# Kernel optimization log

Hardware: AMD Instinct MI355X
Metric: run time of the kernel (lower is better)

The kernel has to match this reference:

```python
import jax, jax.numpy as jnp
import numpy as np

DIM = 1024
HEADS = 16
HEAD_DIM = DIM // HEADS
LAYERS = 8
HIDDEN = 4 * DIM
VOCAB = 266
MAX_POS = 32768
B = 4
L = 2048
SCALE = HEAD_DIM ** -0.5
EPS = 1e-5


def layer_norm(x, g, b):
    m = jnp.mean(x, axis=-1, keepdims=True)
    v = jnp.mean(jnp.square(x - m), axis=-1, keepdims=True)
    return (x - m) * jax.lax.rsqrt(v + EPS) * g + b


def setup_inputs() -> dict:
    key = jax.random.key(0)
    ks = jax.random.split(key, 16)
    s = 0.02
    return {
        "tokens": jax.random.randint(ks[0], (B, L), 0, VOCAB),
        "tok_emb": jax.random.normal(ks[1], (VOCAB, DIM), jnp.float32) * s,
        "pos_emb": jax.random.normal(ks[2], (MAX_POS, DIM), jnp.float32) * s,
        "ln1_g": jnp.ones((LAYERS, DIM), jnp.float32),
        "ln1_b": jnp.zeros((LAYERS, DIM), jnp.float32),
        "q_w": jax.random.normal(ks[3], (LAYERS, DIM, DIM), jnp.float32) * s,
        "k_w": jax.random.normal(ks[4], (LAYERS, DIM, DIM), jnp.float32) * s,
        "v_w": jax.random.normal(ks[5], (LAYERS, DIM, DIM), jnp.float32) * s,
        "o_w": jax.random.normal(ks[6], (LAYERS, DIM, DIM), jnp.float32) * s,
        "ln2_g": jnp.ones((LAYERS, DIM), jnp.float32),
        "ln2_b": jnp.zeros((LAYERS, DIM), jnp.float32),
        "w1_w": jax.random.normal(ks[7], (LAYERS, HIDDEN, DIM), jnp.float32) * s,
        "wg_w": jax.random.normal(ks[8], (LAYERS, HIDDEN, DIM), jnp.float32) * s,
        "w2_w": jax.random.normal(ks[9], (LAYERS, DIM, HIDDEN), jnp.float32) * s,
        "lnf_g": jnp.ones((DIM,), jnp.float32),
        "lnf_b": jnp.zeros((DIM,), jnp.float32),
        "lm_w": jax.random.normal(ks[10], (VOCAB, DIM), jnp.float32) * s,
    }


def reference(tokens, tok_emb, pos_emb, ln1_g, ln1_b, q_w, k_w, v_w, o_w,
              ln2_g, ln2_b, w1_w, wg_w, w2_w, lnf_g, lnf_b, lm_w):
    Bv, Lv = tokens.shape
    x = tok_emb[tokens] + pos_emb[jnp.arange(Lv)][None, :, :]  # [B,L,D]
    # strictly-upper-triangular causal mask (True = masked)
    rows = jnp.arange(Lv)
    mask = rows[None, :] > rows[:, None]  # [L,L], col > row
    pos_bias = jnp.arange(Lv, dtype=x.dtype) * 0.01  # [L]
    neg_inf = jnp.array(-jnp.inf, dtype=x.dtype)

    for i in range(LAYERS):
        h = layer_norm(x, ln1_g[i], ln1_b[i])
        q = jnp.einsum('bld,ed->ble', h, q_w[i]).reshape(Bv, Lv, HEADS, HEAD_DIM).transpose(0, 2, 1, 3)
        k = jnp.einsum('bld,ed->ble', h, k_w[i]).reshape(Bv, Lv, HEADS, HEAD_DIM).transpose(0, 2, 1, 3)
        v = jnp.einsum('bld,ed->ble', h, v_w[i]).reshape(Bv, Lv, HEADS, HEAD_DIM).transpose(0, 2, 1, 3)
        attn = jnp.einsum('bhqd,bhkd->bhqk', q, k) * SCALE
        attn = jnp.where(mask[None, None, :, :], neg_inf, attn)
        attn = attn + pos_bias[None, None, None, :]
        attn = jax.nn.softmax(attn, axis=-1)
        out = jnp.einsum('bhqk,bhkd->bhqd', attn, v).transpose(0, 2, 1, 3).reshape(Bv, Lv, DIM)
        attn_out = jnp.einsum('bld,ed->ble', out, o_w[i])
        x = x + attn_out
        h2 = layer_norm(x, ln2_g[i], ln2_b[i])
        ff = jnp.einsum('blh,dh->bld', jax.nn.silu(jnp.einsum('bld,hd->blh', h2, w1_w[i])) * jnp.einsum('bld,hd->blh', h2, wg_w[i]), w2_w[i])
        x = x + ff

    last = layer_norm(x[:, -1, :], lnf_g, lnf_b)  # [B, D]
    return jnp.einsum('bd,vd->bv', last, lm_w)  # [B, VOCAB]
```

## Files before the change

### kernel.cpp

```cpp
#include <hip/hip_runtime.h>
#include <hip/hip_bf16.h>
#include <math.h>

#define DIMD 1024
#define HEADS 16
#define HD 64
#define LAYERS 8
#define HIDDEN 4096
#define VOCAB 266
#define NB 4
#define SEQ 2048
#define ROWS (NB*SEQ)
#define LOG2E 1.4426950408889634f
#define QSCALE (0.125f * LOG2E)
#define BIAS2 (0.01f * LOG2E)
#define THR2 8.0f

typedef float f32x4 __attribute__((ext_vector_type(4)));
typedef __bf16 bf16x8 __attribute__((ext_vector_type(8)));
typedef __bf16 bf16x4 __attribute__((ext_vector_type(4)));

__device__ __forceinline__ f32x4 mfma16(bf16x8 a, bf16x8 b, f32x4 c) {
    return __builtin_amdgcn_mfma_f32_16x16x32_bf16(a, b, c, 0, 0, 0);
}

__device__ __forceinline__ void gload16(const __bf16* g, __bf16* l) {
    __builtin_amdgcn_global_load_lds(
        (const __attribute__((address_space(1))) void*)g,
        (__attribute__((address_space(3))) void*)l, 16, 0, 0);
}

__global__ void embed_kernel(const int* __restrict__ tok, const float* __restrict__ te,
                             const float* __restrict__ pe, float* __restrict__ x) {
    int row = blockIdx.x;
    int t = tok[row];
    int l = row & (SEQ - 1);
    int c = threadIdx.x;
    f32x4 tv = *(const f32x4*)(te + (size_t)t * DIMD + c * 4);
    f32x4 pv = *(const f32x4*)(pe + (size_t)l * DIMD + c * 4);
    *(f32x4*)(x + (size_t)row * DIMD + c * 4) = tv + pv;
}

__global__ void cvt_kernel(const float* q, const float* k, const float* v, const float* o,
                           const float* w1, const float* wg, const float* w2,
                           __bf16* __restrict__ dst) {
    const size_t MM = 1024 * 1024;
    const float* src; size_t n; size_t off; int ilv = 0;
    switch (blockIdx.y) {
        case 0: src = q;  n = MM;     off = 0;       break;
        case 1: src = k;  n = MM;     off = MM;      break;
        case 2: src = v;  n = MM;     off = 2 * MM;  break;
        case 3: src = o;  n = MM;     off = 3 * MM;  break;
        case 4: src = w1; n = 4 * MM; off = 4 * MM;  ilv = 1; break;
        case 5: src = wg; n = 4 * MM; off = 4 * MM;  ilv = 2; break;
        default: src = w2; n = 4 * MM; off = 12 * MM; break;
    }
    size_t stride = (size_t)gridDim.x * blockDim.x * 8;
    for (size_t i = ((size_t)blockIdx.x * blockDim.x + threadIdx.x) * 8; i < n; i += stride) {
        f32x4 a = *(const f32x4*)(src + i);
        f32x4 b = *(const f32x4*)(src + i + 4);
        bf16x8 ov;
        ov[0] = (__bf16)a[0]; ov[1] = (__bf16)a[1]; ov[2] = (__bf16)a[2]; ov[3] = (__bf16)a[3];
        ov[4] = (__bf16)b[0]; ov[5] = (__bf16)b[1]; ov[6] = (__bf16)b[2]; ov[7] = (__bf16)b[3];
        size_t di;
        if (ilv) {
            size_t row = i >> 10, col = i & 1023;
            di = off + (((row << 1) | (ilv - 1)) << 10) + col;
        } else {
            di = off + i;
        }
        *(bf16x8*)(dst + di) = ov;
    }
}

template<bool F32OUT>
__global__ void ln_kernel(const float* __restrict__ xin, size_t row_stride,
                          const float* __restrict__ g, const float* __restrict__ bb,
                          void* __restrict__ out) {
    int row = blockIdx.x;
    int c = threadIdx.x;
    const float* xr = xin + (size_t)row * row_stride;
    f32x4 v = *(const f32x4*)(xr + c * 4);
    float s = v[0] + v[1] + v[2] + v[3];
    float s2 = v[0]*v[0] + v[1]*v[1] + v[2]*v[2] + v[3]*v[3];
    #pragma unroll
    for (int o = 32; o; o >>= 1) { s += __shfl_xor(s, o); s2 += __shfl_xor(s2, o); }
    __shared__ float red[8];
    int w = c >> 6, lane = c & 63;
    if (lane == 0) { red[w] = s; red[4 + w] = s2; }
    __syncthreads();
    s = red[0] + red[1] + red[2] + red[3];
    s2 = red[4] + red[5] + red[6] + red[7];
    float mean = s * (1.f / DIMD);
    float var = s2 * (1.f / DIMD) - mean * mean;
    float rstd = rsqrtf(var + 1e-5f);
    f32x4 gv = *(const f32x4*)(g + c * 4);
    f32x4 bv = *(const f32x4*)(bb + c * 4);
    f32x4 o4;
    #pragma unroll
    for (int j = 0; j < 4; ++j) o4[j] = (v[j] - mean) * rstd * gv[j] + bv[j];
    if (F32OUT) {
        *(f32x4*)((float*)out + (size_t)row * DIMD + c * 4) = o4;
    } else {
        bf16x4 hv;
        #pragma unroll
        for (int j = 0; j < 4; ++j) hv[j] = (__bf16)o4[j];
        *(bf16x4*)((__bf16*)out + (size_t)row * DIMD + c * 4) = hv;
    }
}

template<int EPI>
__global__ __launch_bounds__(256, 4)
void gemm_bt(const __bf16* __restrict__ A, const __bf16* __restrict__ W,
             int M, int N, int K,
             __bf16* bdst, float* fdst, float scale) {
    __shared__ __bf16 As[128 * 64];
    __shared__ __bf16 Bs[128 * 64];
    int tid = threadIdx.x;
    int lane = tid & 63, w = tid >> 6;
    int wm = w >> 1, wn = w & 1;
    int g16 = lane >> 4, l16 = lane & 15;
    int m0 = blockIdx.y * 128, n0 = blockIdx.x * 128;
    f32x4 acc[4][4] = {};
    int trow = tid >> 3;
    int cs8 = ((tid & 7) ^ (trow & 7)) * 8;
    const __bf16* ga = A + (size_t)(m0 + trow) * K + cs8;
    const __bf16* gb = W + (size_t)(n0 + trow) * K + cs8;
    int xsw = (l16 & 7) << 4;

    for (int k0 = 0; k0 < K; k0 += 64) {
        #pragma unroll
        for (int p = 0; p < 4; ++p) {
            gload16(ga + (size_t)(p * 32) * K + k0, As + (p * 256 + w * 64) * 8);
            gload16(gb + (size_t)(p * 32) * K + k0, Bs + (p * 256 + w * 64) * 8);
        }
        __syncthreads();
        #pragma unroll
        for (int kk = 0; kk < 2; ++kk) {
            bf16x8 af[4], bfv[4];
            #pragma unroll
            for (int f = 0; f < 4; ++f) {
                int ar = wm * 64 + f * 16 + l16;
                int br = wn * 64 + f * 16 + l16;
                af[f]  = *(const bf16x8*)((const char*)As + ((ar * 128 + kk * 64 + g16 * 16) ^ xsw));
                bfv[f] = *(const bf16x8*)((const char*)Bs + ((br * 128 + kk * 64 + g16 * 16) ^ xsw));
            }
            #pragma unroll
            for (int fm = 0; fm < 4; ++fm)
                #pragma unroll
                for (int fn = 0; fn < 4; ++fn)
                    acc[fm][fn] = mfma16(af[fm], bfv[fn], acc[fm][fn]);
        }
        __syncthreads();
    }

    #pragma unroll
    for (int fm = 0; fm < 4; ++fm) {
        int rbase = m0 + wm * 64 + fm * 16 + g16 * 4;
        #pragma unroll
        for (int fn = 0; fn < 4; ++fn) {
            int col = n0 + wn * 64 + fn * 16 + l16;
            if (EPI == 2) {
                #pragma unroll
                for (int j = 0; j < 4; ++j) {
                    size_t idx = (size_t)(rbase + j) * N + col;
                    fdst[idx] += acc[fm][fn][j];
                }
            } else if (EPI == 5) {
                int which = col >> 10;
                int c = col & 1023;
                int hh = c >> 6, d = c & 63;
                if (which == 2) {
                    int b = rbase >> 11, l = rbase & 2047;
                    __bf16* vp = bdst + 2 * (size_t)ROWS * DIMD;
                    bf16x4 hv;
                    #pragma unroll
                    for (int j = 0; j < 4; ++j) hv[j] = (__bf16)acc[fm][fn][j];
                    *(bf16x4*)(vp + ((size_t)(b * HEADS + hh) * HD + d) * SEQ + l) = hv;
                } else {
                    float sc = (which == 0) ? scale : 1.f;
                    __bf16* base = bdst + (size_t)which * ROWS * DIMD;
                    #pragma unroll
                    for (int j = 0; j < 4; ++j) {
                        int row = rbase + j;
                        int b = row >> 11, l = row & 2047;
                        base[(((size_t)(b * HEADS + hh) * SEQ + l) << 6) + d] =
                            (__bf16)(acc[fm][fn][j] * sc);
                    }
                }
            } else if (EPI == 6) {
                #pragma unroll
                for (int j = 0; j < 4; ++j) {
                    float own = acc[fm][fn][j];
                    float other = __shfl_xor(own, 1);
                    if (!(l16 & 1)) {
                        float si = own / (1.f + __expf(-own));
                        bdst[(size_t)(rbase + j) * (N >> 1) + (col >> 1)] = (__bf16)(si * other);
                    }
                }
            }
        }
    }
}

__global__ __launch_bounds__(256, 3)
void attn_kernel(const __bf16* __restrict__ qt, const __bf16* __restrict__ kt,
                 const __bf16* __restrict__ vt, __bf16* __restrict__ ao) {
    int qtile = 15 - (blockIdx.x >> 6);
    int g = blockIdx.x & 63;
    int hh = g & 15, b = g >> 4;
    int tid = threadIdx.x, lane = tid & 63, w = tid >> 6;
    int g16 = lane >> 4, l16 = lane & 15;

    __shared__ __bf16 Ks[2][64 * 64];
    __shared__ __bf16 Vs[2][64 * 64];
    __shared__ __bf16 Ps[4 * 32 * 72];
    __bf16* Pw = Ps + w * (32 * 72);

    const __bf16* qbase = qt + (size_t)(b * HEADS + hh) * SEQ * HD;
    const __bf16* kbase = kt + (size_t)(b * HEADS + hh) * SEQ * HD;
    const __bf16* vbase = vt + (size_t)(b * HEADS + hh) * HD * SEQ;

    int rr = lane >> 3;
    int cs8 = ((lane & 7) ^ rr) * 8;

    int qb = qtile * 128;
    int nt = (qb >> 6) + 2;
    int qrmax = qb + w * 32 + 31;

    bf16x8 qf[2][2];
    #pragma unroll
    for (int rb = 0; rb < 2; ++rb)
        #pragma unroll
        for (int kk = 0; kk < 2; ++kk)
            qf[rb][kk] = *(const bf16x8*)(qbase + (size_t)(qb + w * 32 + rb * 16 + l16) * HD + kk * 32 + g16 * 8);

    f32x4 accO[2][4] = {};
    float mrow[2][4], lrow[2][4];
    #pragma unroll
    for (int rb = 0; rb < 2; ++rb)
        #pragma unroll
        for (int j = 0; j < 4; ++j) { mrow[rb][j] = -1e30f; lrow[rb][j] = 0.f; }

    #pragma unroll
    for (int p = 0; p < 2; ++p) {
        int rbse = p * 32 + w * 8;
        gload16(kbase + (size_t)(rbse + rr) * HD + cs8, Ks[0] + rbse * 64);
        gload16(vbase + (size_t)(rbse + rr) * SEQ + cs8, Vs[0] + rbse * 64);
    }
    __syncthreads();

    for (int t = 0; t < nt; ++t) {
        int cur = t & 1;
        int kv0 = t << 6;

        if (t + 1 < nt) {
            int kv1 = kv0 + 64;
            #pragma unroll
            for (int p = 0; p < 2; ++p) {
                int rbse = p * 32 + w * 8;
                gload16(kbase + (size_t)(kv1 + rbse + rr) * HD + cs8, Ks[cur ^ 1] + rbse * 64);
                gload16(vbase + (size_t)(rbse + rr) * SEQ + kv1 + cs8, Vs[cur ^ 1] + rbse * 64);
            }
        }

        if (kv0 <= qrmax) {
            f32x4 sacc[2][4] = {};
            __builtin_amdgcn_s_setprio(1);
            #pragma unroll
            for (int kk = 0; kk < 2; ++kk) {
                bf16x8 kf[4];
                #pragma unroll
                for (int nk = 0; nk < 4; ++nk) {
                    int key = nk * 16 + l16;
                    int bo = (key * 128 + (kk * 32 + g16 * 8) * 2) ^ ((key & 7) << 4);
                    kf[nk] = *(const bf16x8*)((const char*)Ks[cur] + bo);
                }
                #pragma unroll
                for (int rb = 0; rb < 2; ++rb)
                    #pragma unroll
                    for (int nk = 0; nk < 4; ++nk)
                        sacc[rb][nk] = mfma16(qf[rb][kk], kf[nk], sacc[rb][nk]);
            }
            __builtin_amdgcn_s_setprio(0);

            float mx8[2][4];
            #pragma unroll
            for (int rb = 0; rb < 2; ++rb) {
                #pragma unroll
                for (int j = 0; j < 4; ++j) {
                    int qrow = qb + w * 32 + rb * 16 + g16 * 4 + j;
                    float mx = -1e30f;
                    #pragma unroll
                    for (int nk = 0; nk < 4; ++nk) {
                        int key = kv0 + nk * 16 + l16;
                        float sc = sacc[rb][nk][j];
                        sc = (key <= qrow) ? (sc + BIAS2 * (float)key) : -1e30f;
                        sacc[rb][nk][j] = sc;
                        mx = fmaxf(mx, sc);
                    }
                    mx = fmaxf(mx, __shfl_xor(mx, 1));
                    mx = fmaxf(mx, __shfl_xor(mx, 2));
                    mx = fmaxf(mx, __shfl_xor(mx, 4));
                    mx = fmaxf(mx, __shfl_xor(mx, 8));
                    mx8[rb][j] = mx;
                }
            }

            bool ok = true;
            #pragma unroll
            for (int rb = 0; rb < 2; ++rb)
                #pragma unroll
                for (int j = 0; j < 4; ++j)
                    ok &= (mx8[rb][j] <= mrow[rb][j] + THR2);
            if (!__all(ok)) {
                #pragma unroll
                for (int rb = 0; rb < 2; ++rb) {
                    #pragma unroll
                    for (int j = 0; j < 4; ++j) {
                        float mnew = fmaxf(mrow[rb][j], mx8[rb][j]);
                        float rs = exp2f(mrow[rb][j] - mnew);
                        mrow[rb][j] = mnew;
                        lrow[rb][j] *= rs;
                        #pragma unroll
                        for (int nd = 0; nd < 4; ++nd) accO[rb][nd][j] *= rs;
                    }
                }
            }

            #pragma unroll
            for (int rb = 0; rb < 2; ++rb) {
                #pragma unroll
                for (int j = 0; j < 4; ++j) {
                    float m = mrow[rb][j];
                    float ps = 0.f;
                    #pragma unroll
                    for (int nk = 0; nk < 4; ++nk) {
                        float pp = exp2f(sacc[rb][nk][j] - m);
                        ps += pp;
                        Pw[(rb * 16 + g16 * 4 + j) * 72 + nk * 16 + l16] = (__bf16)pp;
                    }
                    lrow[rb][j] += ps;
                }
            }

            __builtin_amdgcn_s_setprio(1);
            #pragma unroll
            for (int kk = 0; kk < 2; ++kk) {
                bf16x8 pf[2];
                #pragma unroll
                for (int rb = 0; rb < 2; ++rb)
                    pf[rb] = *(const bf16x8*)(Pw + (rb * 16 + l16) * 72 + kk * 32 + g16 * 8);
                #pragma unroll
                for (int nd = 0; nd < 4; ++nd) {
                    int d = nd * 16 + l16;
                    int bo = (d * 128 + (kk * 32 + g16 * 8) * 2) ^ ((d & 7) << 4);
                    bf16x8 vf = *(const bf16x8*)((const char*)Vs[cur] + bo);
                    #pragma unroll
                    for (int rb = 0; rb < 2; ++rb)
                        accO[rb][nd] = mfma16(pf[rb], vf, accO[rb][nd]);
                }
            }
            __builtin_amdgcn_s_setprio(0);
        }
        __syncthreads();
    }

    #pragma unroll
    for (int rb = 0; rb < 2; ++rb) {
        #pragma unroll
        for (int j = 0; j < 4; ++j) {
            float l = lrow[rb][j];
            l += __shfl_xor(l, 1);
            l += __shfl_xor(l, 2);
            l += __shfl_xor(l, 4);
            l += __shfl_xor(l, 8);
            lrow[rb][j] = 1.f / l;
        }
    }
    #pragma unroll
    for (int rb = 0; rb < 2; ++rb)
        #pragma unroll
        for (int nd = 0; nd < 4; ++nd)
            #pragma unroll
            for (int j = 0; j < 4; ++j) {
                int row = qb + w * 32 + rb * 16 + g16 * 4 + j;
                float o = accO[rb][nd][j] * lrow[rb][j];
                ao[(size_t)(b * SEQ + row) * DIMD + hh * HD + nd * 16 + l16] = (__bf16)o;
            }
}

__global__ void lm_head(const float* __restrict__ last, const float* __restrict__ lw,
                        float* __restrict__ out) {
    int v = blockIdx.x;
    int c = threadIdx.x, lane = c & 63, w = c >> 6;
    f32x4 wv = *(const f32x4*)(lw + (size_t)v * DIMD + c * 4);
    float a[NB];
    #pragma unroll
    for (int b = 0; b < NB; ++b) {
        f32x4 xv = *(const f32x4*)(last + b * DIMD + c * 4);
        a[b] = wv[0]*xv[0] + wv[1]*xv[1] + wv[2]*xv[2] + wv[3]*xv[3];
    }
    #pragma unroll
    for (int o = 32; o; o >>= 1)
        #pragma unroll
        for (int b = 0; b < NB; ++b) a[b] += __shfl_xor(a[b], o);
    __shared__ float red[4][NB];
    if (lane == 0)
        #pragma unroll
        for (int b = 0; b < NB; ++b) red[w][b] = a[b];
    __syncthreads();
    if (c < NB) {
        float s = red[0][c] + red[1][c] + red[2][c] + red[3][c];
        out[c * VOCAB + v] = s;
    }
}

extern "C" void kernel_launch(void* const* d_in, const int* in_sizes, int n_in,
                              void* d_out, int out_size, void* d_ws, size_t ws_size,
                              hipStream_t stream) {
    const int*   tokens  = (const int*)d_in[0];
    const float* tok_emb = (const float*)d_in[1];
    const float* pos_emb = (const float*)d_in[2];
    const float* ln1_g   = (const float*)d_in[3];
    const float* ln1_b   = (const float*)d_in[4];
    const float* q_w     = (const float*)d_in[5];
    const float* k_w     = (const float*)d_in[6];
    const float* v_w     = (const float*)d_in[7];
    const float* o_w     = (const float*)d_in[8];
    const float* ln2_g   = (const float*)d_in[9];
    const float* ln2_b   = (const float*)d_in[10];
    const float* w1_w    = (const float*)d_in[11];
    const float* wg_w    = (const float*)d_in[12];
    const float* w2_w    = (const float*)d_in[13];
    const float* lnf_g   = (const float*)d_in[14];
    const float* lnf_b   = (const float*)d_in[15];
    const float* lm_w    = (const float*)d_in[16];

    const size_t MM = 1024 * 1024;
    char* p = (char*)d_ws;
    __bf16* wbf = (__bf16*)p;          p += 16 * MM * 2;
    float*  x   = (float*)p;           p += (size_t)ROWS * DIMD * 4;
    __bf16* h   = (__bf16*)p;          p += (size_t)ROWS * DIMD * 2;
    __bf16* qt  = (__bf16*)p;          p += (size_t)ROWS * DIMD * 2;
    __bf16* kt  = (__bf16*)p;          p += (size_t)ROWS * DIMD * 2;
    __bf16* vt  = (__bf16*)p;          p += (size_t)ROWS * DIMD * 2;
    __bf16* ao  = (__bf16*)p;          p += (size_t)ROWS * DIMD * 2;
    __bf16* abuf= (__bf16*)p;          p += (size_t)ROWS * HIDDEN * 2;
    float*  last= (float*)p;           p += NB * DIMD * 4;

    embed_kernel<<<ROWS, 256, 0, stream>>>(tokens, tok_emb, pos_emb, x);

    for (int i = 0; i < LAYERS; ++i) {
        cvt_kernel<<<dim3(256, 7), 256, 0, stream>>>(
            q_w + (size_t)i * MM, k_w + (size_t)i * MM, v_w + (size_t)i * MM, o_w + (size_t)i * MM,
            w1_w + (size_t)i * 4 * MM, wg_w + (size_t)i * 4 * MM, w2_w + (size_t)i * 4 * MM, wbf);
        __bf16* wqkv = wbf;
        __bf16* wo   = wbf + 3 * MM;
        __bf16* w1g  = wbf + 4 * MM;
        __bf16* w2   = wbf + 12 * MM;

        ln_kernel<false><<<ROWS, 256, 0, stream>>>(x, DIMD, ln1_g + i * DIMD, ln1_b + i * DIMD, h);

        gemm_bt<5><<<dim3(24, 64), 256, 0, stream>>>(h, wqkv, ROWS, 3 * DIMD, DIMD, qt, nullptr, QSCALE);

        attn_kernel<<<1024, 256, 0, stream>>>(qt, kt, vt, ao);

        gemm_bt<2><<<dim3(8, 64), 256, 0, stream>>>(ao, wo, ROWS, DIMD, DIMD, nullptr, x, 1.f);

        ln_kernel<false><<<ROWS, 256, 0, stream>>>(x, DIMD, ln2_g + i * DIMD, ln2_b + i * DIMD, h);

        gemm_bt<6><<<dim3(64, 64), 256, 0, stream>>>(h, w1g, ROWS, 2 * HIDDEN, DIMD, abuf, nullptr, 1.f);

        gemm_bt<2><<<dim3(8, 64), 256, 0, stream>>>(abuf, w2, ROWS, DIMD, HIDDEN, nullptr, x, 1.f);
    }

    ln_kernel<true><<<NB, 256, 0, stream>>>(x + (size_t)(SEQ - 1) * DIMD, (size_t)SEQ * DIMD,
                                            lnf_g, lnf_b, last);
    lm_head<<<VOCAB, 256, 0, stream>>>(last, lm_w, (float*)d_out);
}
```

Measured before the change: 3.827 ms.

## Rewrite attention with transposed 32x32 MFMA, keeping P in registers

The attention kernel now uses 32x32x16 bf16 MFMA and computes S^T (keys x queries), so each lane owns a single query row. Softmax row statistics need only one cross-half shuffle instead of a four-step reduction. The P tile is packed to bf16 and exchanged between wave halves with shuffles rather than written to LDS, and output stores become 4-wide vectors. Occupancy hint drops from 3 to 2 blocks per CU to allow the larger register footprint, and the rest of the model's run time is unchanged.

```diff
diff --git a/kernel.cpp b/kernel.cpp
--- a/kernel.cpp
+++ b/kernel.cpp
@@ -17,11 +17,15 @@
 #define THR2 8.0f
 
 typedef float f32x4 __attribute__((ext_vector_type(4)));
+typedef float f32x16 __attribute__((ext_vector_type(16)));
 typedef __bf16 bf16x8 __attribute__((ext_vector_type(8)));
 typedef __bf16 bf16x4 __attribute__((ext_vector_type(4)));
 
 __device__ __forceinline__ f32x4 mfma16(bf16x8 a, bf16x8 b, f32x4 c) {
     return __builtin_amdgcn_mfma_f32_16x16x32_bf16(a, b, c, 0, 0, 0);
+}
+__device__ __forceinline__ f32x16 mfma32(bf16x8 a, bf16x8 b, f32x16 c) {
+    return __builtin_amdgcn_mfma_f32_32x32x16_bf16(a, b, c, 0, 0, 0);
 }
 
 __device__ __forceinline__ void gload16(const __bf16* g, __bf16* l) {
@@ -29,6 +33,13 @@
         (const __attribute__((address_space(1))) void*)g,
         (__attribute__((address_space(3))) void*)l, 16, 0, 0);
 }
+
+__device__ __forceinline__ unsigned pack2(float a, float b) {
+    union { __bf16 h[2]; unsigned u; } t;
+    t.h[0] = (__bf16)a; t.h[1] = (__bf16)b;
+    return t.u;
+}
+union PUN8 { unsigned u[4]; bf16x8 v; };
 
 __global__ void embed_kernel(const int* __restrict__ tok, const float* __restrict__ te,
                              const float* __restrict__ pe, float* __restrict__ x) {
@@ -203,19 +214,17 @@
     }
 }
 
-__global__ __launch_bounds__(256, 3)
+__global__ __launch_bounds__(256, 2)
 void attn_kernel(const __bf16* __restrict__ qt, const __bf16* __restrict__ kt,
                  const __bf16* __restrict__ vt, __bf16* __restrict__ ao) {
     int qtile = 15 - (blockIdx.x >> 6);
     int g = blockIdx.x & 63;
     int hh = g & 15, b = g >> 4;
     int tid = threadIdx.x, lane = tid & 63, w = tid >> 6;
-    int g16 = lane >> 4, l16 = lane & 15;
+    int l32 = lane & 31, hi = lane >> 5;
 
     __shared__ __bf16 Ks[2][64 * 64];
     __shared__ __bf16 Vs[2][64 * 64];
-    __shared__ __bf16 Ps[4 * 32 * 72];
-    __bf16* Pw = Ps + w * (32 * 72);
 
     const __bf16* qbase = qt + (size_t)(b * HEADS + hh) * SEQ * HD;
     const __bf16* kbase = kt + (size_t)(b * HEADS + hh) * SEQ * HD;
@@ -226,21 +235,16 @@
 
     int qb = qtile * 128;
     int nt = (qb >> 6) + 2;
+    int qrow = qb + w * 32 + l32;
     int qrmax = qb + w * 32 + 31;
 
-    bf16x8 qf[2][2];
-    #pragma unroll
-    for (int rb = 0; rb < 2; ++rb)
-        #pragma unroll
-        for (int kk = 0; kk < 2; ++kk)
-            qf[rb][kk] = *(const bf16x8*)(qbase + (size_t)(qb + w * 32 + rb * 16 + l16) * HD + kk * 32 + g16 * 8);
-
-    f32x4 accO[2][4] = {};
-    float mrow[2][4], lrow[2][4];
-    #pragma unroll
-    for (int rb = 0; rb < 2; ++rb)
-        #pragma unroll
-        for (int j = 0; j < 4; ++j) { mrow[rb][j] = -1e30f; lrow[rb][j] = 0.f; }
+    bf16x8 qf[4];
+    #pragma unroll
+    for (int s = 0; s < 4; ++s)
+        qf[s] = *(const bf16x8*)(qbase + (size_t)qrow * HD + s * 16 + hi * 8);
+
+    f32x16 accO[2] = {};
+    float m = -1e30f, lsum = 0.f;
 
     #pragma unroll
     for (int p = 0; p < 2; ++p) {
@@ -265,129 +269,94 @@
         }
 
         if (kv0 <= qrmax) {
-            f32x4 sacc[2][4] = {};
+            const char* Kb = (const char*)Ks[cur];
+            const char* Vb = (const char*)Vs[cur];
+
+            f32x16 sacc[2] = {};
             __builtin_amdgcn_s_setprio(1);
             #pragma unroll
-            for (int kk = 0; kk < 2; ++kk) {
-                bf16x8 kf[4];
-                #pragma unroll
-                for (int nk = 0; nk < 4; ++nk) {
-                    int key = nk * 16 + l16;
-                    int bo = (key * 128 + (kk * 32 + g16 * 8) * 2) ^ ((key & 7) << 4);
-                    kf[nk] = *(const bf16x8*)((const char*)Ks[cur] + bo);
-                }
-                #pragma unroll
-                for (int rb = 0; rb < 2; ++rb)
+            for (int kb = 0; kb < 2; ++kb) {
+                int row = kb * 32 + l32;
+                int rsw = row & 7;
+                #pragma unroll
+                for (int s = 0; s < 4; ++s) {
+                    int cc = s * 2 + hi;
+                    bf16x8 kf = *(const bf16x8*)(Kb + row * 128 + ((cc ^ rsw) << 4));
+                    sacc[kb] = mfma32(kf, qf[s], sacc[kb]);
+                }
+            }
+            __builtin_amdgcn_s_setprio(0);
+
+            float mx = -1e30f;
+            #pragma unroll
+            for (int kb = 0; kb < 2; ++kb)
+                #pragma unroll
+                for (int r = 0; r < 16; ++r) {
+                    int key = kv0 + kb * 32 + (r & 3) + 8 * (r >> 2) + 4 * hi;
+                    float v = sacc[kb][r];
+                    v = (key <= qrow) ? (v + BIAS2 * (float)key) : -1e30f;
+                    sacc[kb][r] = v;
+                    mx = fmaxf(mx, v);
+                }
+            mx = fmaxf(mx, __shfl_xor(mx, 32));
+
+            if (!__all(mx <= m + THR2)) {
+                float mnew = fmaxf(m, mx);
+                float rs = exp2f(m - mnew);
+                m = mnew; lsum *= rs;
+                #pragma unroll
+                for (int f = 0; f < 2; ++f)
                     #pragma unroll
-                    for (int nk = 0; nk < 4; ++nk)
-                        sacc[rb][nk] = mfma16(qf[rb][kk], kf[nk], sacc[rb][nk]);
-            }
-            __builtin_amdgcn_s_setprio(0);
-
-            float mx8[2][4];
-            #pragma unroll
-            for (int rb = 0; rb < 2; ++rb) {
-                #pragma unroll
-                for (int j = 0; j < 4; ++j) {
-                    int qrow = qb + w * 32 + rb * 16 + g16 * 4 + j;
-                    float mx = -1e30f;
+                    for (int r = 0; r < 16; ++r) accO[f][r] *= rs;
+            }
+
+            #pragma unroll
+            for (int kb = 0; kb < 2; ++kb) {
+                float p[16];
+                #pragma unroll
+                for (int r = 0; r < 16; ++r) { p[r] = exp2f(sacc[kb][r] - m); lsum += p[r]; }
+                #pragma unroll
+                for (int s = 0; s < 2; ++s) {
+                    unsigned a0 = pack2(p[s*8+0], p[s*8+1]);
+                    unsigned a1 = pack2(p[s*8+2], p[s*8+3]);
+                    unsigned b0 = pack2(p[s*8+4], p[s*8+5]);
+                    unsigned b1 = pack2(p[s*8+6], p[s*8+7]);
+                    unsigned xa0 = (unsigned)__shfl_xor((int)a0, 32);
+                    unsigned xa1 = (unsigned)__shfl_xor((int)a1, 32);
+                    unsigned xb0 = (unsigned)__shfl_xor((int)b0, 32);
+                    unsigned xb1 = (unsigned)__shfl_xor((int)b1, 32);
+                    PUN8 pf;
+                    pf.u[0] = hi ? xb0 : a0;
+                    pf.u[1] = hi ? xb1 : a1;
+                    pf.u[2] = hi ? b0  : xa0;
+                    pf.u[3] = hi ? b1  : xa1;
+                    __builtin_amdgcn_s_setprio(1);
                     #pragma unroll
-                    for (int nk = 0; nk < 4; ++nk) {
-                        int key = kv0 + nk * 16 + l16;
-                        float sc = sacc[rb][nk][j];
-                        sc = (key <= qrow) ? (sc + BIAS2 * (float)key) : -1e30f;
-                        sacc[rb][nk][j] = sc;
-                        mx = fmaxf(mx, sc);
+                    for (int f = 0; f < 2; ++f) {
+                        int d = f * 32 + l32;
+                        int cc = kb * 4 + s * 2 + hi;
+                        bf16x8 vf = *(const bf16x8*)(Vb + d * 128 + ((cc ^ (d & 7)) << 4));
+                        accO[f] = mfma32(vf, pf.v, accO[f]);
                     }
-                    mx = fmaxf(mx, __shfl_xor(mx, 1));
-                    mx = fmaxf(mx, __shfl_xor(mx, 2));
-                    mx = fmaxf(mx, __shfl_xor(mx, 4));
-                    mx = fmaxf(mx, __shfl_xor(mx, 8));
-                    mx8[rb][j] = mx;
-                }
-            }
-
-            bool ok = true;
-            #pragma unroll
-            for (int rb = 0; rb < 2; ++rb)
-                #pragma unroll
-                for (int j = 0; j < 4; ++j)
-                    ok &= (mx8[rb][j] <= mrow[rb][j] + THR2);
-            if (!__all(ok)) {
-                #pragma unroll
-                for (int rb = 0; rb < 2; ++rb) {
-                    #pragma unroll
-                    for (int j = 0; j < 4; ++j) {
-                        float mnew = fmaxf(mrow[rb][j], mx8[rb][j]);
-                        float rs = exp2f(mrow[rb][j] - mnew);
-                        mrow[rb][j] = mnew;
-                        lrow[rb][j] *= rs;
-                        #pragma unroll
-                        for (int nd = 0; nd < 4; ++nd) accO[rb][nd][j] *= rs;
-                    }
-                }
-            }
-
-            #pragma unroll
-            for (int rb = 0; rb < 2; ++rb) {
-                #pragma unroll
-                for (int j = 0; j < 4; ++j) {
-                    float m = mrow[rb][j];
-                    float ps = 0.f;
-                    #pragma unroll
-                    for (int nk = 0; nk < 4; ++nk) {
-                        float pp = exp2f(sacc[rb][nk][j] - m);
-                        ps += pp;
-                        Pw[(rb * 16 + g16 * 4 + j) * 72 + nk * 16 + l16] = (__bf16)pp;
-                    }
-                    lrow[rb][j] += ps;
-                }
-            }
-
-            __builtin_amdgcn_s_setprio(1);
-            #pragma unroll
-            for (int kk = 0; kk < 2; ++kk) {
-                bf16x8 pf[2];
-                #pragma unroll
-                for (int rb = 0; rb < 2; ++rb)
-                    pf[rb] = *(const bf16x8*)(Pw + (rb * 16 + l16) * 72 + kk * 32 + g16 * 8);
-                #pragma unroll
-                for (int nd = 0; nd < 4; ++nd) {
-                    int d = nd * 16 + l16;
-                    int bo = (d * 128 + (kk * 32 + g16 * 8) * 2) ^ ((d & 7) << 4);
-                    bf16x8 vf = *(const bf16x8*)((const char*)Vs[cur] + bo);
-                    #pragma unroll
-                    for (int rb = 0; rb < 2; ++rb)
-                        accO[rb][nd] = mfma16(pf[rb], vf, accO[rb][nd]);
-                }
-            }
-            __builtin_amdgcn_s_setprio(0);
+                    __builtin_amdgcn_s_setprio(0);
+                }
+            }
         }
         __syncthreads();
     }
 
-    #pragma unroll
-    for (int rb = 0; rb < 2; ++rb) {
-        #pragma unroll
-        for (int j = 0; j < 4; ++j) {
-            float l = lrow[rb][j];
-            l += __shfl_xor(l, 1);
-            l += __shfl_xor(l, 2);
-            l += __shfl_xor(l, 4);
-            l += __shfl_xor(l, 8);
-            lrow[rb][j] = 1.f / l;
-        }
-    }
-    #pragma unroll
-    for (int rb = 0; rb < 2; ++rb)
-        #pragma unroll
-        for (int nd = 0; nd < 4; ++nd)
-            #pragma unroll
-            for (int j = 0; j < 4; ++j) {
-                int row = qb + w * 32 + rb * 16 + g16 * 4 + j;
-                float o = accO[rb][nd][j] * lrow[rb][j];
-                ao[(size_t)(b * SEQ + row) * DIMD + hh * HD + nd * 16 + l16] = (__bf16)o;
-            }
+    lsum += __shfl_xor(lsum, 32);
+    float inv = 1.f / lsum;
+    #pragma unroll
+    for (int f = 0; f < 2; ++f)
+        #pragma unroll
+        for (int gI = 0; gI < 4; ++gI) {
+            bf16x4 hv;
+            #pragma unroll
+            for (int j = 0; j < 4; ++j) hv[j] = (__bf16)(accO[f][gI * 4 + j] * inv);
+            int d = f * 32 + 8 * gI + 4 * hi;
+            *(bf16x4*)(ao + (size_t)(b * SEQ + qrow) * DIMD + hh * HD + d) = hv;
+        }
 }
 
 __global__ void lm_head(const float* __restrict__ last, const float* __restrict__ lw,
```

Result: no change. 3.772 ms (median of 2 runs) (-1.4%).
